# Optimization experiments

Measured on AMD Instinct MI355X. Metric: run time of the kernel, lower is better.

Reference implementation:

```python
import jax, jax.numpy as jnp
import numpy as np

N, D_MODEL, D_PE, H = 4096, 512, 16, 8


def setup_inputs() -> dict:
    key = jax.random.key(0)
    ks = jax.random.split(key, 6)
    s = 1.0 / np.sqrt(D_MODEL)
    return {
        "x": jax.random.normal(ks[0], (N, D_MODEL), dtype=jnp.float32),
        "pe": jax.random.normal(ks[1], (N, D_PE), dtype=jnp.float32),
        "w_qkv": jax.random.normal(ks[2], (D_MODEL, 3 * D_MODEL), dtype=jnp.float32) * s,
        "b_qkv": jnp.zeros((3 * D_MODEL,), dtype=jnp.float32),
        "w_pe": jax.random.normal(ks[3], (D_PE, H), dtype=jnp.float32) * (1.0 / np.sqrt(D_PE)),
        "b_pe": jnp.zeros((H,), dtype=jnp.float32),
        "w_out": jax.random.normal(ks[4], (D_MODEL, D_MODEL), dtype=jnp.float32) * s,
        "b_out": jnp.zeros((D_MODEL,), dtype=jnp.float32),
    }


def reference(x, pe, w_qkv, b_qkv, w_pe, b_pe, w_out, b_out):
    n, d = x.shape
    h = w_pe.shape[1]
    hd = d // h
    scale = hd ** -0.5

    qkv = (x @ w_qkv + b_qkv).reshape(n, 3, h, hd)  # [N,3,H,hd]
    q = jnp.transpose(qkv[:, 0], (1, 0, 2))  # [H,N,hd]
    k = jnp.transpose(qkv[:, 1], (1, 0, 2))
    v = jnp.transpose(qkv[:, 2], (1, 0, 2))

    pe_proj = pe @ w_pe + b_pe  # [N,H]
    # bias[h,i,j] = pe_proj[j,h] - pe_proj[i,h]  (matches torch unsqueeze/permute)
    pt = pe_proj.T  # [H,N]
    bias = pt[:, None, :] - pt[:, :, None]  # [H,N,N]

    scores = jnp.einsum('hnd,hmd->hnm', q, k) * scale + bias  # [H,N,N]
    attn = jax.nn.softmax(scores, axis=-1)
    out = jnp.einsum('hnm,hmd->hnd', attn, v)  # [H,N,hd]
    out = jnp.transpose(out, (1, 0, 2)).reshape(n, d)
    return out @ w_out + b_out
```

## Files before the change

kernel.cpp:

```cpp
#include <hip/hip_runtime.h>
#include <stdint.h>
#include <stddef.h>


typedef unsigned short u16;
typedef __attribute__((ext_vector_type(8))) short short8;
typedef __attribute__((ext_vector_type(8))) unsigned short us8;
typedef __attribute__((ext_vector_type(4))) unsigned short us4;
typedef __attribute__((ext_vector_type(4))) float floatx4;

__device__ __forceinline__ u16 f2b(float f) {
  union { float f; uint32_t u; } v; v.f = f;
  uint32_t u = v.u;
  return (u16)((u + 0x7fffu + ((u >> 16) & 1u)) >> 16);
}

__device__ __forceinline__ uint32_t pkbf16(float a, float b) {
  union { float f; uint32_t u; } x, y; x.f = a; y.f = b;
  return __builtin_amdgcn_perm(y.u + 0x8000u, x.u + 0x8000u, 0x07060302u);
}

#if __has_builtin(__builtin_amdgcn_exp2f)
__device__ __forceinline__ float fexp2(float x) { return __builtin_amdgcn_exp2f(x); }
#else
__device__ __forceinline__ float fexp2(float x) { return exp2f(x); }
#endif

__device__ __forceinline__ void gld16(const u16* g, u16* l) {
  __builtin_amdgcn_global_load_lds(
      (const __attribute__((address_space(1))) uint32_t*)(const void*)g,
      (__attribute__((address_space(3))) uint32_t*)(void*)l, 16, 0, 0);
}


__device__ __forceinline__ void tr_tile(const float* __restrict__ in,
                                        u16* __restrict__ out, int R, int C,
                                        int bx, int by, u16 (*tile)[33]) {
  int tx = threadIdx.x & 31, ty = threadIdx.x >> 5;
  int c0 = bx * 32, r0 = by * 32;
#pragma unroll
  for (int i = 0; i < 32; i += 8)
    tile[ty + i][tx] = f2b(in[(size_t)(r0 + ty + i) * C + c0 + tx]);
  __syncthreads();
#pragma unroll
  for (int i = 0; i < 32; i += 8)
    out[(size_t)(c0 + ty + i) * R + r0 + tx] = tile[tx][ty + i];
}

__global__ __launch_bounds__(256) void k_prep(
    const float* __restrict__ x, u16* __restrict__ xb,
    const float* __restrict__ w_qkv, u16* __restrict__ wqkvT,
    const float* __restrict__ w_out, u16* __restrict__ woutT,
    const float* __restrict__ pe, const float* __restrict__ w_pe,
    const float* __restrict__ b_pe, float* __restrict__ wexp,
    u16* __restrict__ wpb) {
  __shared__ u16 tile[32][33];
  int b = blockIdx.x;
  if (b < 2048) {
    int i = b * 256 + threadIdx.x;
    float4 v = ((const float4*)x)[i];
    uint2 o = make_uint2(pkbf16(v.x, v.y), pkbf16(v.z, v.w));
    ((uint2*)xb)[i] = o;
  } else if (b < 2816) {
    int idx = b - 2048;
    tr_tile(w_qkv, wqkvT, 512, 1536, idx % 48, idx / 48, tile);
  } else if (b < 3072) {
    int idx = b - 2816;
    tr_tile(w_out, woutT, 512, 512, idx % 16, idx / 16, tile);
  } else {
    int idx = (b - 3072) * 256 + threadIdx.x;
    int h = idx >> 12, n = idx & 4095;
    float acc = b_pe[h];
#pragma unroll
    for (int d = 0; d < 16; ++d) acc = fmaf(pe[n * 16 + d], w_pe[d * 8 + h], acc);
    float w = exp2f(acc * 1.4426950408889634f - 16.0f);
    u16 wb = f2b(w);
    union { uint32_t u; float f; } cv; cv.u = ((uint32_t)wb) << 16;
    wexp[h * 4096 + n] = cv.f;
    int pn = (n & ~31) | (((n >> 2) & 3) << 3) | (((n >> 4) & 1) << 2) | (n & 3);
    wpb[h * 4096 + pn] = wb;
  }
}


__global__ __launch_bounds__(512, 6) void k_gemm_qkv(const u16* __restrict__ A,
                                                     const u16* __restrict__ Bt,
                                                     const float* __restrict__ bias,
                                                     const float* __restrict__ wexp,
                                                     u16* __restrict__ qk,
                                                     u16* __restrict__ vtp) {
  __shared__ __align__(16) u16 smem[24576];
  const int tid = threadIdx.x;
  const int lane = tid & 63, wave = tid >> 6;
  const int colx = lane & 15, quad = lane >> 4;
  const int m0 = blockIdx.y * 64, n0 = blockIdx.x * 128;
  const int wm = wave >> 2, wn = wave & 3;
  const int sc = (lane & 7) ^ ((lane >> 3) & 7);
  const floatx4 fz = {0.f, 0.f, 0.f, 0.f};
  floatx4 acc[2][2];
#pragma unroll
  for (int i = 0; i < 2; ++i)
#pragma unroll
    for (int j = 0; j < 2; ++j) acc[i][j] = fz;

#define PREF_QKV(k0, b)                                                       \
  {                                                                           \
    int rowa = wave * 8 + (lane >> 3);                                        \
    gld16(&A[(size_t)(m0 + rowa) * 512 + (k0) + sc * 8],                      \
          &smem[(b) * 4096 + wave * 512 + lane * 8]);                         \
    _Pragma("unroll") for (int c = 0; c < 2; ++c) {                           \
      int rowb = wave * 16 + c * 8 + (lane >> 3);                             \
      gld16(&Bt[(size_t)(n0 + rowb) * 512 + (k0) + sc * 8],                   \
            &smem[8192 + (b) * 8192 + wave * 1024 + c * 512 + lane * 8]);     \
    }                                                                         \
  }

  PREF_QKV(0, 0);
  __syncthreads();
  for (int it = 0; it < 8; ++it) {
    int cur = it & 1;
    if (it < 7) PREF_QKV((it + 1) * 64, cur ^ 1);
    const u16* As = &smem[cur * 4096];
    const u16* Bs = &smem[8192 + cur * 8192];
#pragma unroll
    for (int kk = 0; kk < 2; ++kk) {
      short8 af[2], bf[2];
#pragma unroll
      for (int i = 0; i < 2; ++i) {
        int row = wm * 32 + i * 16 + colx;
        af[i] = *(const short8*)&As[row * 64 + (((kk * 4 + quad) ^ (colx & 7))) * 8];
      }
#pragma unroll
      for (int j = 0; j < 2; ++j) {
        int row = wn * 32 + j * 16 + colx;
        bf[j] = *(const short8*)&Bs[row * 64 + (((kk * 4 + quad) ^ (colx & 7))) * 8];
      }
#pragma unroll
      for (int i = 0; i < 2; ++i)
#pragma unroll
        for (int j = 0; j < 2; ++j)
          acc[i][j] = __builtin_amdgcn_mfma_f32_16x16x32_bf16(af[i], bf[j], acc[i][j], 0, 0, 0);
    }
    __syncthreads();
  }

  const bool isV = (blockIdx.x >= 8);
  if (!isV) {
#pragma unroll
    for (int j = 0; j < 2; ++j) {
      int c = n0 + wn * 32 + j * 16 + colx;
      float bq = bias[c];
      float qs = (c < 512) ? 0.18033688011112042f : 1.0f;
#pragma unroll
      for (int i = 0; i < 2; ++i)
#pragma unroll
        for (int r = 0; r < 4; ++r) {
          int row = m0 + wm * 32 + i * 16 + quad * 4 + r;
          qk[(size_t)row * 1024 + c] = f2b((acc[i][j][r] + bq) * qs);
        }
    }
  } else {
    const int dv = n0 - 1024;
    u16* Vl = smem;
    const int hh = (dv + wn * 32) >> 6;
#pragma unroll
    for (int j = 0; j < 2; ++j) {
      float bq = bias[n0 + wn * 32 + j * 16 + colx];
#pragma unroll
      for (int i = 0; i < 2; ++i) {
        floatx4 wv = *(const floatx4*)&wexp[hh * 4096 + m0 + wm * 32 + i * 16 + quad * 4];
        us4 o;
#pragma unroll
        for (int r = 0; r < 4; ++r) o[r] = f2b((acc[i][j][r] + bq) * wv[r]);
        int dl = wn * 32 + j * 16 + colx;
        int nc = wm * 32 + quad * 8 + i * 4;
        *(us4*)&Vl[dl * 72 + nc] = o;
      }
    }
    __syncthreads();
#pragma unroll
    for (int t = 0; t < 2; ++t) {
      int idx = t * 512 + tid;
      int dl = idx >> 3, ch = idx & 7;
      *(us8*)&vtp[(size_t)(dv + dl) * 4096 + m0 + ch * 8] =
          *(const us8*)&Vl[dl * 72 + ch * 8];
    }
  }
#undef PREF_QKV
}


__global__ __launch_bounds__(256, 4) void k_flash(const u16* __restrict__ qk,
                                                  const u16* __restrict__ vt,
                                                  const u16* __restrict__ wpb,
                                                  float* __restrict__ opart,
                                                  float* __restrict__ lpart) {
  __shared__ __align__(16) u16 smem[20480];
  float* bufs = (float*)smem;

  const int tid = threadIdx.x;
  const int lane = tid & 63, wave = tid >> 6;
  const int colx = lane & 15, quad = lane >> 4;
  const int ih = wave >> 1, jq = wave & 1;
  const int q0 = blockIdx.x * 64;
  const int h = blockIdx.y;
  const int z = blockIdx.z;
  const int kvb = z * 2048;
  const floatx4 fz = {0.f, 0.f, 0.f, 0.f};

  const int sc = (lane & 7) ^ ((lane >> 3) & 7);
  const int srow = wave * 16 + (lane >> 3);

#pragma unroll
  for (int t = 0; t < 2; ++t) {
    int idx = t * 256 + tid;
    int row = idx >> 3, ch = idx & 7;
    *(us8*)&smem[row * 64 + (ch ^ (row & 7)) * 8] =
        *(const us8*)&qk[(size_t)(q0 + row) * 1024 + h * 64 + ch * 8];
  }
  const u16* qptr = qk + (size_t)(kvb + srow) * 1024 + 512 + h * 64 + sc * 8;
  const u16* vptr = vt + (size_t)(h * 64 + srow) * 4096 + kvb + sc * 8;
  const u16* wptr = wpb + h * 4096 + kvb + jq * 32 + quad * 8;
  gld16(qptr, &smem[4096 + wave * 1024 + lane * 8]);
  gld16(qptr + 8192, &smem[4096 + wave * 1024 + 512 + lane * 8]);
  gld16(vptr, &smem[12288 + wave * 1024 + lane * 8]);
  gld16(vptr + 32768, &smem[12288 + wave * 1024 + 512 + lane * 8]);
  qptr += 65536;
  vptr += 64;
  __syncthreads();

  short8 qf[2][2];
#pragma unroll
  for (int iq = 0; iq < 2; ++iq)
#pragma unroll
    for (int kk = 0; kk < 2; ++kk) {
      int row = ih * 32 + iq * 16 + colx;
      qf[iq][kk] = *(const short8*)&smem[row * 64 + (((kk * 4 + quad) ^ (colx & 7))) * 8];
    }

  floatx4 oacc[2][4], lacc[2];
  lacc[0] = fz; lacc[1] = fz;
#pragma unroll
  for (int iq = 0; iq < 2; ++iq)
#pragma unroll
    for (int cb = 0; cb < 4; ++cb) oacc[iq][cb] = fz;

#define FBODY(CUR, PREF)                                                      \
  {                                                                           \
    short8 wf = *(const short8*)wptr;                                         \
    wptr += 64;                                                               \
    if (PREF) {                                                               \
      gld16(qptr, &smem[4096 + (1 - (CUR)) * 4096 + wave * 1024 + lane * 8]); \
      gld16(qptr + 8192,                                                      \
            &smem[4096 + (1 - (CUR)) * 4096 + wave * 1024 + 512 + lane * 8]); \
      gld16(vptr, &smem[12288 + (1 - (CUR)) * 4096 + wave * 1024 + lane * 8]);\
      gld16(vptr + 32768,                                                     \
            &smem[12288 + (1 - (CUR)) * 4096 + wave * 1024 + 512 + lane * 8]);\
      qptr += 65536;                                                          \
      vptr += 64;                                                             \
    }                                                                         \
    const u16* Ks = &smem[4096 + (CUR) * 4096];                               \
    const u16* Vts = &smem[12288 + (CUR) * 4096];                             \
    floatx4 sacc[2][2] = {{fz, fz}, {fz, fz}};                                \
    _Pragma("unroll") for (int j2 = 0; j2 < 2; ++j2) {                        \
      _Pragma("unroll") for (int kk = 0; kk < 2; ++kk) {                      \
        int row = jq * 32 + j2 * 16 + colx;                                   \
        short8 kf = *(const short8*)&Ks[row * 64 +                            \
                                        (((kk * 4 + quad) ^ (colx & 7))) * 8];\
        sacc[0][j2] = __builtin_amdgcn_mfma_f32_16x16x32_bf16(                \
            kf, qf[0][kk], sacc[0][j2], 0, 0, 0);                             \
        sacc[1][j2] = __builtin_amdgcn_mfma_f32_16x16x32_bf16(                \
            kf, qf[1][kk], sacc[1][j2], 0, 0, 0);                             \
      }                                                                       \
    }                                                                         \
    union { uint32_t w[4]; short8 s; } pk[2];                                 \
    _Pragma("unroll") for (int iq = 0; iq < 2; ++iq) {                        \
      _Pragma("unroll") for (int j2 = 0; j2 < 2; ++j2) {                      \
        float p0 = fexp2(sacc[iq][j2][0]);                                    \
        float p1 = fexp2(sacc[iq][j2][1]);                                    \
        float p2 = fexp2(sacc[iq][j2][2]);                                    \
        float p3 = fexp2(sacc[iq][j2][3]);                                    \
        pk[iq].w[j2 * 2 + 0] = pkbf16(p0, p1);                                \
        pk[iq].w[j2 * 2 + 1] = pkbf16(p2, p3);                                \
      }                                                                       \
    }                                                                         \
    _Pragma("unroll") for (int cb = 0; cb < 4; ++cb) {                        \
      int row = cb * 16 + colx;                                               \
      short8 vf = *(const short8*)&Vts[row * 64 +                             \
                                       (((jq * 4 + quad) ^ (colx & 7))) * 8]; \
      oacc[0][cb] = __builtin_amdgcn_mfma_f32_16x16x32_bf16(                  \
          pk[0].s, vf, oacc[0][cb], 0, 0, 0);                                 \
      oacc[1][cb] = __builtin_amdgcn_mfma_f32_16x16x32_bf16(                  \
          pk[1].s, vf, oacc[1][cb], 0, 0, 0);                                 \
    }                                                                         \
    lacc[0] = __builtin_amdgcn_mfma_f32_16x16x32_bf16(pk[0].s, wf, lacc[0], 0, 0, 0); \
    lacc[1] = __builtin_amdgcn_mfma_f32_16x16x32_bf16(pk[1].s, wf, lacc[1], 0, 0, 0); \
    __syncthreads();                                                          \
  }

  for (int t = 0; t < 15; ++t) {
    FBODY(0, 1)
    FBODY(1, 1)
  }
  FBODY(0, 1)
  FBODY(1, 0)
#undef FBODY

  float* b = bufs + ih * 2080;
  if (jq == 1) {
#pragma unroll
    for (int iq = 0; iq < 2; ++iq)
#pragma unroll
      for (int cb = 0; cb < 4; ++cb)
#pragma unroll
        for (int r = 0; r < 4; ++r)
          b[(iq * 16 + quad * 4 + r) * 65 + cb * 16 + colx] = oacc[iq][cb][r];
    if (colx == 0)
#pragma unroll
      for (int iq = 0; iq < 2; ++iq)
#pragma unroll
        for (int r = 0; r < 4; ++r) b[(iq * 16 + quad * 4 + r) * 65 + 64] = lacc[iq][r];
  }
  __syncthreads();
  if (jq == 0) {
#pragma unroll
    for (int iq = 0; iq < 2; ++iq) {
#pragma unroll
      for (int cb = 0; cb < 4; ++cb)
#pragma unroll
        for (int r = 0; r < 4; ++r)
          oacc[iq][cb][r] += b[(iq * 16 + quad * 4 + r) * 65 + cb * 16 + colx];
#pragma unroll
      for (int r = 0; r < 4; ++r) lacc[iq][r] += b[(iq * 16 + quad * 4 + r) * 65 + 64];
    }
    float* op = opart + (size_t)z * 2097152;
#pragma unroll
    for (int iq = 0; iq < 2; ++iq)
#pragma unroll
      for (int cb = 0; cb < 4; ++cb)
#pragma unroll
        for (int r = 0; r < 4; ++r)
          op[(size_t)(q0 + ih * 32 + iq * 16 + quad * 4 + r) * 512 + h * 64 + cb * 16 + colx] =
              oacc[iq][cb][r];
    if (colx == 0)
#pragma unroll
      for (int iq = 0; iq < 2; ++iq)
#pragma unroll
        for (int r = 0; r < 4; ++r)
          lpart[z * 32768 + h * 4096 + q0 + ih * 32 + iq * 16 + quad * 4 + r] = lacc[iq][r];
  }
}


__global__ __launch_bounds__(256) void k_comb(const float* __restrict__ opart,
                                              const float* __restrict__ lpart,
                                              u16* __restrict__ ao) {
  int idx = blockIdx.x * 256 + threadIdx.x;
  int n = idx >> 7, d4 = idx & 127;
  int h = d4 >> 4;
  float l = lpart[h * 4096 + n] + lpart[32768 + h * 4096 + n];
  float inv = 1.0f / l;
  float4 o0 = *(const float4*)&opart[(size_t)n * 512 + d4 * 4];
  float4 o1 = *(const float4*)&opart[2097152 + (size_t)n * 512 + d4 * 4];
  us4 o;
  o[0] = f2b((o0.x + o1.x) * inv);
  o[1] = f2b((o0.y + o1.y) * inv);
  o[2] = f2b((o0.z + o1.z) * inv);
  o[3] = f2b((o0.w + o1.w) * inv);
  *(us4*)&ao[(size_t)n * 512 + d4 * 4] = o;
}


__global__ __launch_bounds__(512, 4) void k_gemm_out(const u16* __restrict__ A,
                                                     const u16* __restrict__ Bt,
                                                     const float* __restrict__ bias,
                                                     float* __restrict__ Cout) {
  __shared__ __align__(16) u16 smem[16384];
  const int tid = threadIdx.x;
  const int lane = tid & 63, wave = tid >> 6;
  const int colx = lane & 15, quad = lane >> 4;
  const int m0 = blockIdx.y * 64, n0 = blockIdx.x * 64;
  const int wm = wave >> 2, wn = wave & 3;
  const int sc = (lane & 7) ^ ((lane >> 3) & 7);
  const floatx4 fz = {0.f, 0.f, 0.f, 0.f};
  floatx4 acc[2];
  acc[0] = fz; acc[1] = fz;

#define PREF_OUT(k0, b)                                                       \
  {                                                                           \
    int rowa = wave * 8 + (lane >> 3);                                        \
    gld16(&A[(size_t)(m0 + rowa) * 512 + (k0) + sc * 8],                      \
          &smem[(b) * 4096 + wave * 512 + lane * 8]);                         \
    gld16(&Bt[(size_t)(n0 + rowa) * 512 + (k0) + sc * 8],                     \
          &smem[8192 + (b) * 4096 + wave * 512 + lane * 8]);                  \
  }

  PREF_OUT(0, 0);
  __syncthreads();
  for (int it = 0; it < 8; ++it) {
    int cur = it & 1;
    if (it < 7) PREF_OUT((it + 1) * 64, cur ^ 1);
    const u16* As = &smem[cur * 4096];
    const u16* Bs = &smem[8192 + cur * 4096];
#pragma unroll
    for (int kk = 0; kk < 2; ++kk) {
      short8 af[2], bf;
#pragma unroll
      for (int i = 0; i < 2; ++i) {
        int row = wm * 32 + i * 16 + colx;
        af[i] = *(const short8*)&As[row * 64 + (((kk * 4 + quad) ^ (colx & 7))) * 8];
      }
      {
        int row = wn * 16 + colx;
        bf = *(const short8*)&Bs[row * 64 + (((kk * 4 + quad) ^ (colx & 7))) * 8];
      }
#pragma unroll
      for (int i = 0; i < 2; ++i)
        acc[i] = __builtin_amdgcn_mfma_f32_16x16x32_bf16(af[i], bf, acc[i], 0, 0, 0);
    }
    __syncthreads();
  }
  int c = n0 + wn * 16 + colx;
  float bq = bias[c];
#pragma unroll
  for (int i = 0; i < 2; ++i)
#pragma unroll
    for (int r = 0; r < 4; ++r) {
      int row = m0 + wm * 32 + i * 16 + quad * 4 + r;
      Cout[(size_t)row * 512 + c] = acc[i][r] + bq;
    }
#undef PREF_OUT
}


extern "C" void kernel_launch(void* const* d_in, const int* in_sizes, int n_in,
                              void* d_out, int out_size, void* d_ws, size_t ws_size,
                              hipStream_t stream) {
  const float* x     = (const float*)d_in[0];
  const float* pe    = (const float*)d_in[1];
  const float* w_qkv = (const float*)d_in[2];
  const float* b_qkv = (const float*)d_in[3];
  const float* w_pe  = (const float*)d_in[4];
  const float* b_pe  = (const float*)d_in[5];
  const float* w_out = (const float*)d_in[6];
  const float* b_out = (const float*)d_in[7];
  float* out = (float*)d_out;

  u16* xb    = (u16*)d_ws;
  u16* wqkvT = xb    + 2097152;
  u16* woutT = wqkvT + 786432;
  u16* qk    = woutT + 262144;
  u16* vt    = qk    + 4194304;
  u16* wpb   = vt    + 2097152;
  u16* ao    = wpb   + 32768;
  float* wexp  = (float*)(ao + 2097152);
  float* opart = wexp + 32768;
  float* lpart = opart + 4194304;

  k_prep<<<3200, 256, 0, stream>>>(x, xb, w_qkv, wqkvT, w_out, woutT,
                                   pe, w_pe, b_pe, wexp, wpb);
  k_gemm_qkv<<<dim3(12, 64), 512, 0, stream>>>(xb, wqkvT, b_qkv, wexp, qk, vt);
  k_flash<<<dim3(64, 8, 2), 256, 0, stream>>>(qk, vt, wpb, opart, lpart);
  k_comb<<<2048, 256, 0, stream>>>(opart, lpart, ao);
  k_gemm_out<<<dim3(8, 64), 512, 0, stream>>>(ao, woutT, b_out, out);
}
```

Measured before the change: 143.8 us.

## Drop split-KV in flash kernel and fuse normalization, removing combine kernel

The flash attention kernel no longer splits the key/value range across two z-blocks. Each block now walks all 4096 keys and normalizes its output in-register before writing bf16 directly. This removes the combine kernel, its launch, and the fp32 partial-output round trip through memory. In exchange the grid shrinks from 1024 to 512 blocks and each block's serial loop doubles, which may underfill the GPU's compute units.

```diff
diff --git a/kernel.cpp b/kernel.cpp
--- a/kernel.cpp
+++ b/kernel.cpp
@@ -193,8 +193,7 @@
 __global__ __launch_bounds__(256, 4) void k_flash(const u16* __restrict__ qk,
                                                   const u16* __restrict__ vt,
                                                   const u16* __restrict__ wpb,
-                                                  float* __restrict__ opart,
-                                                  float* __restrict__ lpart) {
+                                                  u16* __restrict__ ao) {
   __shared__ __align__(16) u16 smem[20480];
   float* bufs = (float*)smem;
 
@@ -204,8 +203,6 @@
   const int ih = wave >> 1, jq = wave & 1;
   const int q0 = blockIdx.x * 64;
   const int h = blockIdx.y;
-  const int z = blockIdx.z;
-  const int kvb = z * 2048;
   const floatx4 fz = {0.f, 0.f, 0.f, 0.f};
 
   const int sc = (lane & 7) ^ ((lane >> 3) & 7);
@@ -218,9 +215,9 @@
     *(us8*)&smem[row * 64 + (ch ^ (row & 7)) * 8] =
         *(const us8*)&qk[(size_t)(q0 + row) * 1024 + h * 64 + ch * 8];
   }
-  const u16* qptr = qk + (size_t)(kvb + srow) * 1024 + 512 + h * 64 + sc * 8;
-  const u16* vptr = vt + (size_t)(h * 64 + srow) * 4096 + kvb + sc * 8;
-  const u16* wptr = wpb + h * 4096 + kvb + jq * 32 + quad * 8;
+  const u16* qptr = qk + (size_t)srow * 1024 + 512 + h * 64 + sc * 8;
+  const u16* vptr = vt + (size_t)(h * 64 + srow) * 4096 + sc * 8;
+  const u16* wptr = wpb + h * 4096 + jq * 32 + quad * 8;
   gld16(qptr, &smem[4096 + wave * 1024 + lane * 8]);
   gld16(qptr + 8192, &smem[4096 + wave * 1024 + 512 + lane * 8]);
   gld16(vptr, &smem[12288 + wave * 1024 + lane * 8]);
@@ -298,7 +295,7 @@
     __syncthreads();                                                          \
   }
 
-  for (int t = 0; t < 15; ++t) {
+  for (int t = 0; t < 31; ++t) {
     FBODY(0, 1)
     FBODY(1, 1)
   }
@@ -333,41 +330,21 @@
 #pragma unroll
       for (int r = 0; r < 4; ++r) lacc[iq][r] += b[(iq * 16 + quad * 4 + r) * 65 + 64];
     }
-    float* op = opart + (size_t)z * 2097152;
-#pragma unroll
-    for (int iq = 0; iq < 2; ++iq)
+#pragma unroll
+    for (int iq = 0; iq < 2; ++iq) {
+      float inv[4];
+#pragma unroll
+      for (int r = 0; r < 4; ++r) inv[r] = 1.0f / lacc[iq][r];
 #pragma unroll
       for (int cb = 0; cb < 4; ++cb)
 #pragma unroll
-        for (int r = 0; r < 4; ++r)
-          op[(size_t)(q0 + ih * 32 + iq * 16 + quad * 4 + r) * 512 + h * 64 + cb * 16 + colx] =
-              oacc[iq][cb][r];
-    if (colx == 0)
-#pragma unroll
-      for (int iq = 0; iq < 2; ++iq)
-#pragma unroll
-        for (int r = 0; r < 4; ++r)
-          lpart[z * 32768 + h * 4096 + q0 + ih * 32 + iq * 16 + quad * 4 + r] = lacc[iq][r];
-  }
-}
-
-
-__global__ __launch_bounds__(256) void k_comb(const float* __restrict__ opart,
-                                              const float* __restrict__ lpart,
-                                              u16* __restrict__ ao) {
-  int idx = blockIdx.x * 256 + threadIdx.x;
-  int n = idx >> 7, d4 = idx & 127;
-  int h = d4 >> 4;
-  float l = lpart[h * 4096 + n] + lpart[32768 + h * 4096 + n];
-  float inv = 1.0f / l;
-  float4 o0 = *(const float4*)&opart[(size_t)n * 512 + d4 * 4];
-  float4 o1 = *(const float4*)&opart[2097152 + (size_t)n * 512 + d4 * 4];
-  us4 o;
-  o[0] = f2b((o0.x + o1.x) * inv);
-  o[1] = f2b((o0.y + o1.y) * inv);
-  o[2] = f2b((o0.z + o1.z) * inv);
-  o[3] = f2b((o0.w + o1.w) * inv);
-  *(us4*)&ao[(size_t)n * 512 + d4 * 4] = o;
+        for (int r = 0; r < 4; ++r) {
+          int row = q0 + ih * 32 + iq * 16 + quad * 4 + r;
+          ao[(size_t)row * 512 + h * 64 + cb * 16 + colx] =
+              f2b(oacc[iq][cb][r] * inv[r]);
+        }
+    }
+  }
 }
 
 
@@ -454,13 +431,10 @@
   u16* wpb   = vt    + 2097152;
   u16* ao    = wpb   + 32768;
   float* wexp  = (float*)(ao + 2097152);
-  float* opart = wexp + 32768;
-  float* lpart = opart + 4194304;
 
   k_prep<<<3200, 256, 0, stream>>>(x, xb, w_qkv, wqkvT, w_out, woutT,
                                    pe, w_pe, b_pe, wexp, wpb);
   k_gemm_qkv<<<dim3(12, 64), 512, 0, stream>>>(xb, wqkvT, b_qkv, wexp, qk, vt);
-  k_flash<<<dim3(64, 8, 2), 256, 0, stream>>>(qk, vt, wpb, opart, lpart);
-  k_comb<<<2048, 256, 0, stream>>>(opart, lpart, ao);
+  k_flash<<<dim3(64, 8), 256, 0, stream>>>(qk, vt, wpb, ao);
   k_gemm_out<<<dim3(8, 64), 512, 0, stream>>>(ao, woutT, b_out, out);
 }
```

New measurement: 137.7 us. -4.2%, faster.
